# Kernel tuning notes

Measured on AMD Instinct MI355X. Metric: run time of the kernel, lower is better.

Reference implementation:

```python
import jax, jax.numpy as jnp
import numpy as np

SEQ_LEN = 512
MAX_SPAN = 15
BATCH = 8
HIDDEN = 1024
WIDTH_DIM = 64
NUM_LABELS = 3


def _enumerate_spans(seq_len, max_span):
    starts, ends = [], []
    for s in range(seq_len):
        for e in range(s, min(s + max_span, seq_len)):
            starts.append(s)
            ends.append(e)
    return np.asarray(starts, np.int32), np.asarray(ends, np.int32)


def setup_inputs() -> dict:
    key = jax.random.key(0)
    k = jax.random.split(key, 6)
    starts, ends = _enumerate_spans(SEQ_LEN, MAX_SPAN)  # N = 7575
    d_in = HIDDEN * 2 + WIDTH_DIM  # 2112
    return {
        "sequence_output": jax.random.normal(k[0], (BATCH, SEQ_LEN, HIDDEN), jnp.float32),
        "width_emb": jax.random.normal(k[1], (MAX_SPAN, WIDTH_DIM), jnp.float32) * 0.02,
        "W1": jax.random.normal(k[2], (d_in, HIDDEN), jnp.float32) * (1.0 / np.sqrt(d_in)),
        "b1": jnp.zeros((HIDDEN,), jnp.float32),
        "W2": jax.random.normal(k[3], (HIDDEN, NUM_LABELS), jnp.float32) * (1.0 / np.sqrt(HIDDEN)),
        "b2": jnp.zeros((NUM_LABELS,), jnp.float32),
        "span_starts": jnp.asarray(starts),
        "span_ends": jnp.asarray(ends),
    }


def reference(sequence_output, width_emb, W1, b1, W2, b2, span_starts, span_ends):
    # Gather start/end token representations for every candidate span.
    B = sequence_output.shape[0]
    N = span_starts.shape[0]
    start_repr = sequence_output[:, span_starts]            # [B, N, H]
    end_repr = sequence_output[:, span_ends]                # [B, N, H]
    width_repr = width_emb[span_ends - span_starts]         # [N, 64]
    width_repr = jnp.broadcast_to(width_repr[None], (B, N, width_repr.shape[-1]))
    span_reprs = jnp.concatenate([start_repr, end_repr, width_repr], axis=-1)  # [B, N, 2H+64]
    # Span classifier MLP (dropout is identity in eval mode).
    h = jax.nn.relu(jnp.einsum("bnd,dh->bnh", span_reprs, W1) + b1)
    logits = jnp.einsum("bnh,hl->bnl", h, W2) + b2          # [B, N, num_labels]
    return logits
```

## Files before the change

kernel.cpp:

```cpp
#include <hip/hip_runtime.h>
#include <stdint.h>

#define SEQ 512
#define BATCH 8
#define HID 1024

typedef __attribute__((ext_vector_type(8))) __bf16 bf16x8;
typedef __attribute__((ext_vector_type(4))) float f32x4;

__device__ __forceinline__ unsigned short f2bf(float f) {
    unsigned int u = __float_as_uint(f);
    unsigned int r = 0x7fffu + ((u >> 16) & 1u);
    return (unsigned short)((u + r) >> 16);
}

__device__ __forceinline__ void unpack8(uint4 v, float* f) {
    f[0] = __uint_as_float(v.x << 16);
    f[1] = __uint_as_float(v.x & 0xffff0000u);
    f[2] = __uint_as_float(v.y << 16);
    f[3] = __uint_as_float(v.y & 0xffff0000u);
    f[4] = __uint_as_float(v.z << 16);
    f[5] = __uint_as_float(v.z & 0xffff0000u);
    f[6] = __uint_as_float(v.w << 16);
    f[7] = __uint_as_float(v.w & 0xffff0000u);
}

__global__ __launch_bounds__(256) void k_prep(const float* __restrict__ seq,
                                              const float* __restrict__ wemb,
                                              const float* __restrict__ W1,
                                              const float* __restrict__ b1,
                                              ushort* __restrict__ seqb,
                                              ushort* __restrict__ Bt,
                                              ushort* __restrict__ Rbf) {
    __shared__ float tile[32][33];
    const int bid = blockIdx.x;
    const int tid = threadIdx.x;
    if (bid < 4096) {
        int i = bid * 256 + tid;
        float4 v = ((const float4*)seq)[i];
        ushort4 o;
        o.x = f2bf(v.x); o.y = f2bf(v.y); o.z = f2bf(v.z); o.w = f2bf(v.w);
        ((ushort4*)seqb)[i] = o;
    } else if (bid < 6144) {
        int idx = bid - 4096;
        int nb = (idx & 63) * 32, kb = (idx >> 6) * 32;
        int tx = tid & 31, ty = tid >> 5;
        int n = nb + tx;
        int rb = (n < 1024) ? 0 : 1024;
        int nc = n - rb;
#pragma unroll
        for (int i = 0; i < 4; ++i) {
            int k = kb + ty + i * 8;
            tile[ty + i * 8][tx] = W1[(size_t)(rb + k) * 1024 + nc];
        }
        __syncthreads();
#pragma unroll
        for (int i = 0; i < 4; ++i) {
            int n2 = nb + ty + i * 8;
            Bt[(size_t)n2 * 1024 + kb + tx] = f2bf(tile[tx][ty + i * 8]);
        }
    } else {
        int idx = (bid - 6144) * 256 + tid;
        int w = idx >> 10, j = idx & 1023;
        float acc = b1[j];
#pragma unroll
        for (int c = 0; c < 64; ++c)
            acc = fmaf(wemb[w * 64 + c], W1[(size_t)(2048 + c) * 1024 + j], acc);
        Rbf[idx] = f2bf(acc);
    }
}

__global__ __launch_bounds__(256) void k_gemm(const ushort* __restrict__ A,
                                              const ushort* __restrict__ Bt,
                                              ushort* __restrict__ P,
                                              ushort* __restrict__ Q) {
    __shared__ ushort Al[2][8192];
    __shared__ ushort Bl[2][8192];
    const int tid = threadIdx.x;
    const int wid = tid >> 6;
    const int lane = tid & 63;
    const int bid = blockIdx.x;
    const int x = bid & 7, t8 = bid >> 3;
    const int m0 = (((x >> 1) << 3) + (t8 >> 3)) * 128;
    const int n0 = (((x & 1) << 3) + (t8 & 7)) * 128;
    const int wm = (wid >> 1) * 64;
    const int wn = (wid & 1) * 64;
    const int srow = lane >> 2;
    const int scol = (lane & 3) * 8;
    const int fr = lane & 15;
    const int fk = (lane >> 4) * 8;

    f32x4 acc[4][4] = {};

    const ushort* Abase = A  + (size_t)(m0 + srow) * 1024 + scol;
    const ushort* Bbase = Bt + (size_t)(n0 + srow) * 1024 + scol;

#define STAGE(buf, k0)                                                                     \
    {                                                                                      \
        _Pragma("unroll")                                                                  \
        for (int r = 0; r < 4; ++r) {                                                      \
            int c = wid + 4 * r;                                          \
            int half = c >> 3;                                  \
            int rows = (c & 7) * 16;                                     \
            const ushort* sa = Abase + (size_t)rows * 1024 + (k0) + half * 32;             \
            const ushort* sb = Bbase + (size_t)rows * 1024 + (k0) + half * 32;             \
            int loff = half * 4096 + rows * 32;                                            \
            __builtin_amdgcn_global_load_lds((const __attribute__((address_space(1))) void*)sa, \
                                             (__attribute__((address_space(3))) void*)(&Al[buf][loff]), \
                                             16, 0, 0);                                    \
            __builtin_amdgcn_global_load_lds((const __attribute__((address_space(1))) void*)sb, \
                                             (__attribute__((address_space(3))) void*)(&Bl[buf][loff]), \
                                             16, 0, 0);                                    \
        }                                                                                  \
    }

#define COMPUTE(cur)                                                                       \
    {                                                                                      \
        _Pragma("unroll")                                                                  \
        for (int kk = 0; kk < 2; ++kk) {                                                   \
            bf16x8 af[4], bg[4];                                                           \
            _Pragma("unroll")                                                              \
            for (int i = 0; i < 4; ++i)                                                    \
                af[i] = *(const bf16x8*)(&Al[cur][kk * 4096 + (wm + i * 16 + fr) * 32 + fk]); \
            _Pragma("unroll")                                                              \
            for (int j = 0; j < 4; ++j)                                                    \
                bg[j] = *(const bf16x8*)(&Bl[cur][kk * 4096 + (wn + j * 16 + fr) * 32 + fk]); \
            __builtin_amdgcn_s_setprio(1);                                                 \
            _Pragma("unroll")                                                              \
            for (int i = 0; i < 4; ++i)                                                    \
                _Pragma("unroll")                                                          \
                for (int j = 0; j < 4; ++j)                                                \
                    acc[i][j] = __builtin_amdgcn_mfma_f32_16x16x32_bf16(af[i], bg[j], acc[i][j], 0, 0, 0); \
            __builtin_amdgcn_s_setprio(0);                                                 \
        }                                                                                  \
    }

    STAGE(0, 0);
    for (int t = 0; t < 15; ++t) {
        const int cur = t & 1;
        STAGE(cur ^ 1, (t + 1) * 64);
        asm volatile("s_waitcnt vmcnt(8)" ::: "memory");
        __builtin_amdgcn_s_barrier();
        COMPUTE(cur);
        __builtin_amdgcn_s_barrier();
    }
    asm volatile("s_waitcnt vmcnt(0)" ::: "memory");
    __builtin_amdgcn_s_barrier();
    COMPUTE(1);
#undef STAGE
#undef COMPUTE

    ushort* Cb = (n0 < 1024) ? P : Q;
    const int nc0 = n0 & 1023;
    const int cr = (lane >> 4) * 4;
    const int cc = lane & 15;
#pragma unroll
    for (int i = 0; i < 4; ++i)
#pragma unroll
        for (int j = 0; j < 4; ++j) {
            ushort* Cp = Cb + (size_t)(m0 + wm + i * 16 + cr) * 1024 + (nc0 + wn + j * 16 + cc);
#pragma unroll
            for (int r = 0; r < 4; ++r)
                Cp[(size_t)r * 1024] = f2bf(acc[i][j][r]);
        }
}

__global__ __launch_bounds__(1024) void k_span2(const ushort* __restrict__ Pmat,
                                                const ushort* __restrict__ Qmat,
                                                const ushort* __restrict__ Rbf,
                                                const float* __restrict__ W2,
                                                const float* __restrict__ b2,
                                                float* __restrict__ out, int nspans) {
    __shared__ ushort Qs[30 * 1024];
    __shared__ ushort Rs[15 * 1024];
    const int tid = threadIdx.x;
    const int wid = tid >> 6, lane = tid & 63;
    const int b = blockIdx.x >> 5;
    const int s0 = (blockIdx.x & 31) << 4;

#pragma unroll
    for (int i = 0; i < 4; ++i) {
        int c = wid + (i << 4);
        if (c < 60) {
            int g = (c << 9) + lane * 8;
            int row = s0 + (g >> 10);
            if (row > SEQ - 1) row = SEQ - 1;
            const ushort* src = Qmat + (((size_t)(b << 9) + row) << 10) + (g & 1023);
            __builtin_amdgcn_global_load_lds((const __attribute__((address_space(1))) void*)src,
                                             (__attribute__((address_space(3))) void*)(Qs + (c << 9)),
                                             16, 0, 0);
        }
    }
#pragma unroll
    for (int i = 0; i < 2; ++i) {
        int c = wid + (i << 4);
        if (c < 30) {
            int g = (c << 9) + lane * 8;
            __builtin_amdgcn_global_load_lds((const __attribute__((address_space(1))) void*)(Rbf + g),
                                             (__attribute__((address_space(3))) void*)(Rs + (c << 9)),
                                             16, 0, 0);
        }
    }

    float w2r[3][2][8];
#pragma unroll
    for (int it = 0; it < 2; ++it)
#pragma unroll
        for (int u = 0; u < 8; ++u) {
            int j = lane * 8 + it * 512 + u;
            w2r[0][it][u] = W2[j * 3 + 0];
            w2r[1][it][u] = W2[j * 3 + 1];
            w2r[2][it][u] = W2[j * 3 + 2];
        }
    const float bb0 = b2[0], bb1 = b2[1], bb2 = b2[2];

    const int s = s0 + wid;
    float pf[16];
    {
        const uint4* pr = (const uint4*)(Pmat + (((size_t)(b << 9) + s) << 10) + lane * 8);
        unpack8(pr[0], pf);
        unpack8(pr[64], pf + 8);
    }

    __syncthreads();

    const int rrem = SEQ - s;
    const int nsp = (rrem < 15) ? rrem : 15;
    const int off = (rrem >= 15) ? 15 * s : (7575 - (rrem * (rrem + 1)) / 2);
    float* op = out + ((size_t)b * nspans + off) * 3;

    for (int w = 0; w < nsp; ++w) {
        const int erow = wid + w;
        float a0 = 0.f, a1 = 0.f, a2 = 0.f;
#pragma unroll
        for (int it = 0; it < 2; ++it) {
            uint4 qv = *(const uint4*)((const char*)Qs + erow * 2048 + it * 1024 + lane * 16);
            uint4 rv = *(const uint4*)((const char*)Rs + w * 2048 + it * 1024 + lane * 16);
            float qf[8], rf[8];
            unpack8(qv, qf);
            unpack8(rv, rf);
#pragma unroll
            for (int u = 0; u < 8; ++u) {
                float h = pf[it * 8 + u] + qf[u] + rf[u];
                h = fmaxf(h, 0.f);
                a0 = fmaf(h, w2r[0][it][u], a0);
                a1 = fmaf(h, w2r[1][it][u], a1);
                a2 = fmaf(h, w2r[2][it][u], a2);
            }
        }
#pragma unroll
        for (int o = 32; o; o >>= 1) {
            a0 += __shfl_xor(a0, o);
            a1 += __shfl_xor(a1, o);
            a2 += __shfl_xor(a2, o);
        }
        if (lane == 0) {
            op[w * 3 + 0] = a0 + bb0;
            op[w * 3 + 1] = a1 + bb1;
            op[w * 3 + 2] = a2 + bb2;
        }
    }
}

extern "C" void kernel_launch(void* const* d_in, const int* in_sizes, int n_in,
                              void* d_out, int out_size, void* d_ws, size_t ws_size,
                              hipStream_t stream) {
    const float* seq    = (const float*)d_in[0];
    const float* wemb   = (const float*)d_in[1];
    const float* W1     = (const float*)d_in[2];
    const float* b1     = (const float*)d_in[3];
    const float* W2     = (const float*)d_in[4];
    const float* b2     = (const float*)d_in[5];
    float* out = (float*)d_out;
    int nspans = in_sizes[6];

    char* ws = (char*)d_ws;
    ushort* seqb = (ushort*)ws;
    ushort* Bt   = (ushort*)(ws + (8u << 20));
    ushort* Pmat = (ushort*)(ws + (12u << 20));
    ushort* Qmat = (ushort*)(ws + (20u << 20));
    ushort* Rbf  = (ushort*)(ws + (28u << 20));

    hipLaunchKernelGGL(k_prep, dim3(6204), dim3(256), 0, stream,
                       seq, wemb, W1, b1, seqb, Bt, Rbf);
    hipLaunchKernelGGL(k_gemm, dim3(512), dim3(256), 0, stream, seqb, Bt, Pmat, Qmat);
    hipLaunchKernelGGL(k_span2, dim3(BATCH * (SEQ / 16)), dim3(1024), 0, stream,
                       Pmat, Qmat, Rbf, W2, b2, out, nspans);
}
```

Before: 60.86 us.

## Shrink span blocks to 8 starts and pre-transpose W2 for vector loads

The span-scoring kernel now uses 512-thread blocks that each handle 8 start positions instead of 16. Each block stages 22 Q rows instead of 30 in shared memory, so more blocks can be resident per CU (launch bounds 512,4) and the grid doubles to 512 blocks. W2 is transposed into a label-major fp32 buffer inside the prep kernel, so the span kernel can read its weights with float4 loads instead of strided scalar loads. The cost is more redundant Q and R staging per span, since the halo rows are now shared by fewer starts, plus a few extra prep blocks.

```diff
diff --git a/kernel.cpp b/kernel.cpp
--- a/kernel.cpp
+++ b/kernel.cpp
@@ -29,9 +29,11 @@
                                               const float* __restrict__ wemb,
                                               const float* __restrict__ W1,
                                               const float* __restrict__ b1,
+                                              const float* __restrict__ W2,
                                               ushort* __restrict__ seqb,
                                               ushort* __restrict__ Bt,
-                                              ushort* __restrict__ Rbf) {
+                                              ushort* __restrict__ Rbf,
+                                              float* __restrict__ W2t) {
     __shared__ float tile[32][33];
     const int bid = blockIdx.x;
     const int tid = threadIdx.x;
@@ -59,7 +61,7 @@
             int n2 = nb + ty + i * 8;
             Bt[(size_t)n2 * 1024 + kb + tx] = f2bf(tile[tx][ty + i * 8]);
         }
-    } else {
+    } else if (bid < 6204) {
         int idx = (bid - 6144) * 256 + tid;
         int w = idx >> 10, j = idx & 1023;
         float acc = b1[j];
@@ -67,6 +69,10 @@
         for (int c = 0; c < 64; ++c)
             acc = fmaf(wemb[w * 64 + c], W1[(size_t)(2048 + c) * 1024 + j], acc);
         Rbf[idx] = f2bf(acc);
+    } else {
+        int idx = (bid - 6204) * 256 + tid;
+        int l = idx >> 10, j = idx & 1023;
+        W2t[idx] = W2[j * 3 + l];
     }
 }
 
@@ -99,9 +105,9 @@
     {                                                                                      \
         _Pragma("unroll")                                                                  \
         for (int r = 0; r < 4; ++r) {                                                      \
-            int c = wid + 4 * r;                                          \
-            int half = c >> 3;                                  \
-            int rows = (c & 7) * 16;                                     \
+            int c = wid + 4 * r;                                                           \
+            int half = c >> 3;                                                             \
+            int rows = (c & 7) * 16;                                                       \
             const ushort* sa = Abase + (size_t)rows * 1024 + (k0) + half * 32;             \
             const ushort* sb = Bbase + (size_t)rows * 1024 + (k0) + half * 32;             \
             int loff = half * 4096 + rows * 32;                                            \
@@ -165,23 +171,23 @@
         }
 }
 
-__global__ __launch_bounds__(1024) void k_span2(const ushort* __restrict__ Pmat,
-                                                const ushort* __restrict__ Qmat,
-                                                const ushort* __restrict__ Rbf,
-                                                const float* __restrict__ W2,
-                                                const float* __restrict__ b2,
-                                                float* __restrict__ out, int nspans) {
-    __shared__ ushort Qs[30 * 1024];
+__global__ __launch_bounds__(512, 4) void k_span2(const ushort* __restrict__ Pmat,
+                                                  const ushort* __restrict__ Qmat,
+                                                  const ushort* __restrict__ Rbf,
+                                                  const float* __restrict__ W2t,
+                                                  const float* __restrict__ b2,
+                                                  float* __restrict__ out, int nspans) {
+    __shared__ ushort Qs[22 * 1024];
     __shared__ ushort Rs[15 * 1024];
     const int tid = threadIdx.x;
     const int wid = tid >> 6, lane = tid & 63;
-    const int b = blockIdx.x >> 5;
-    const int s0 = (blockIdx.x & 31) << 4;
-
-#pragma unroll
-    for (int i = 0; i < 4; ++i) {
-        int c = wid + (i << 4);
-        if (c < 60) {
+    const int b = blockIdx.x >> 6;
+    const int s0 = (blockIdx.x & 63) << 3;
+
+#pragma unroll
+    for (int i = 0; i < 6; ++i) {
+        int c = wid + (i << 3);
+        if (c < 44) {
             int g = (c << 9) + lane * 8;
             int row = s0 + (g >> 10);
             if (row > SEQ - 1) row = SEQ - 1;
@@ -192,8 +198,8 @@
         }
     }
 #pragma unroll
-    for (int i = 0; i < 2; ++i) {
-        int c = wid + (i << 4);
+    for (int i = 0; i < 4; ++i) {
+        int c = wid + (i << 3);
         if (c < 30) {
             int g = (c << 9) + lane * 8;
             __builtin_amdgcn_global_load_lds((const __attribute__((address_space(1))) void*)(Rbf + g),
@@ -204,13 +210,15 @@
 
     float w2r[3][2][8];
 #pragma unroll
-    for (int it = 0; it < 2; ++it)
-#pragma unroll
-        for (int u = 0; u < 8; ++u) {
-            int j = lane * 8 + it * 512 + u;
-            w2r[0][it][u] = W2[j * 3 + 0];
-            w2r[1][it][u] = W2[j * 3 + 1];
-            w2r[2][it][u] = W2[j * 3 + 2];
+    for (int l = 0; l < 3; ++l)
+#pragma unroll
+        for (int it = 0; it < 2; ++it) {
+            const float4* p = (const float4*)(W2t + l * 1024 + it * 512 + lane * 8);
+            float4 v0 = p[0], v1 = p[1];
+            w2r[l][it][0] = v0.x; w2r[l][it][1] = v0.y;
+            w2r[l][it][2] = v0.z; w2r[l][it][3] = v0.w;
+            w2r[l][it][4] = v1.x; w2r[l][it][5] = v1.y;
+            w2r[l][it][6] = v1.z; w2r[l][it][7] = v1.w;
         }
     const float bb0 = b2[0], bb1 = b2[1], bb2 = b2[2];
 
@@ -280,10 +288,11 @@
     ushort* Pmat = (ushort*)(ws + (12u << 20));
     ushort* Qmat = (ushort*)(ws + (20u << 20));
     ushort* Rbf  = (ushort*)(ws + (28u << 20));
-
-    hipLaunchKernelGGL(k_prep, dim3(6204), dim3(256), 0, stream,
-                       seq, wemb, W1, b1, seqb, Bt, Rbf);
+    float*  W2t  = (float*)(ws + (29u << 20));
+
+    hipLaunchKernelGGL(k_prep, dim3(6216), dim3(256), 0, stream,
+                       seq, wemb, W1, b1, W2, seqb, Bt, Rbf, W2t);
     hipLaunchKernelGGL(k_gemm, dim3(512), dim3(256), 0, stream, seqb, Bt, Pmat, Qmat);
-    hipLaunchKernelGGL(k_span2, dim3(BATCH * (SEQ / 16)), dim3(1024), 0, stream,
-                       Pmat, Qmat, Rbf, W2, b2, out, nspans);
-}
+    hipLaunchKernelGGL(k_span2, dim3(BATCH * 64), dim3(512), 0, stream,
+                       Pmat, Qmat, Rbf, W2t, b2, out, nspans);
+}
```

Measured after the change: 60.33 us. About the same (-0.9%).
